# Kernel tuning notes

Measured on AMD Instinct MI355X. Metric: run time of the kernel, lower is better.

## Reference

```python
import jax, jax.numpy as jnp
import numpy as np

D_MODEL = 1024
NUM_HEADS = 16
D_K = D_MODEL // NUM_HEADS  # 64


def _xavier(key, shape):
    fan_in, fan_out = shape[-1], shape[-2]
    limit = float(np.sqrt(6.0 / (fan_in + fan_out)))
    return jax.random.uniform(key, shape, jnp.float32, -limit, limit)


def setup_inputs() -> dict:
    key = jax.random.key(0)
    kx, kq, kk, kv, ko = jax.random.split(key, 5)
    x = jax.random.normal(kx, (2, 2048, D_MODEL), dtype=jnp.float32)
    q_heads = _xavier(kq, (NUM_HEADS, D_K, D_MODEL))
    k_heads = _xavier(kk, (NUM_HEADS, D_K, D_MODEL))
    v_heads = _xavier(kv, (NUM_HEADS, D_K, D_MODEL))
    output_proj = _xavier(ko, (D_MODEL, NUM_HEADS * D_K))
    return {"x": x, "q_heads": q_heads, "k_heads": k_heads,
            "v_heads": v_heads, "output_proj": output_proj}


def reference(x, q_heads, k_heads, v_heads, output_proj):
    # x: [b, s, d]; q/k/v_heads: [h, dk, d]; output_proj: [d, h*dk]
    b, s, d = x.shape
    h, dk, _ = q_heads.shape
    scale = 1.0 / jnp.sqrt(jnp.asarray(dk, x.dtype))
    # per-head projections: [b, h, s, dk]
    Q = jnp.einsum('bsd,hkd->bhsk', x, q_heads)
    K = jnp.einsum('bsd,hkd->bhsk', x, k_heads)
    V = jnp.einsum('bsd,hkd->bhsk', x, v_heads)
    scores = jnp.einsum('bhqk,bhsk->bhqs', Q, K) * scale  # [b,h,s,s]
    causal = jnp.tril(jnp.ones((s, s), dtype=bool))       # True where allowed
    scores = jnp.where(causal, scores, -jnp.inf)
    attn = jax.nn.softmax(scores, axis=-1)
    out = jnp.einsum('bhqs,bhsk->bhqk', attn, V)           # [b,h,s,dk]
    out = out.transpose(0, 2, 1, 3).reshape(b, s, h * dk)  # [b,s,h*dk]
    return jnp.einsum('bsk,dk->bsd', out, output_proj)
```

## Files before the change

### kernel.cpp

```cpp
#include <hip/hip_runtime.h>
#include <hip/hip_bf16.h>
#include <math.h>

#define D_MODEL 1024
#define NHEADS  16
#define DK      64
#define SEQ     2048
#define KDIM    1024

typedef __bf16 bf16x8 __attribute__((ext_vector_type(8)));
typedef short  s16x4  __attribute__((ext_vector_type(4)));
typedef float  f32x4  __attribute__((ext_vector_type(4)));

__device__ __forceinline__ void gload16(const void* g, void* l) {
    __builtin_amdgcn_global_load_lds(
        (const __attribute__((address_space(1))) void*)g,
        (__attribute__((address_space(3))) void*)l, 16, 0, 0);
}

__device__ __forceinline__ unsigned short f2bf(float f) {
    __hip_bfloat16 h = __float2bfloat16(f);
    return *(unsigned short*)&h;
}

__device__ __forceinline__ unsigned pk2bf(float a, float b) {
    __hip_bfloat162 h = __float22bfloat162_rn(make_float2(a, b));
    return *(unsigned*)&h;
}

#define QSCALE 0.18033688011112042f

__global__ __launch_bounds__(256) void cast_kernel(
    const float* __restrict__ x,
    const float* __restrict__ qw,
    const float* __restrict__ kw,
    const float* __restrict__ vw,
    const float* __restrict__ wo,
    unsigned short* __restrict__ xb,
    unsigned short* __restrict__ wqkv,
    unsigned short* __restrict__ wob)
{
    const size_t t = (size_t)blockIdx.x * 256 + threadIdx.x;
    const size_t X4 = 1048576;
    const size_t W4 = 262144;

    const float* src;
    unsigned short* dst;
    size_t o;
    if (t < X4)            { src = x;  dst = xb;             o = t; }
    else if (t < X4 + W4)  { src = qw; dst = wqkv;           o = t - X4; }
    else if (t < X4 + 2*W4){ src = kw; dst = wqkv + 1048576; o = t - X4 - W4; }
    else if (t < X4 + 3*W4){ src = vw; dst = wqkv + 2097152; o = t - X4 - 2*W4; }
    else                   { src = wo; dst = wob;            o = t - X4 - 3*W4; }

    float4 v = ((const float4*)src)[o];
    ushort4 r;
    r.x = f2bf(v.x); r.y = f2bf(v.y); r.z = f2bf(v.z); r.w = f2bf(v.w);
    ((ushort4*)dst)[o] = r;
}

__global__ __launch_bounds__(256) void mfma_gemm_qkv(
    const unsigned short* __restrict__ A,
    const unsigned short* __restrict__ B,
    unsigned short* __restrict__ Qb,
    unsigned short* __restrict__ Kb,
    unsigned short* __restrict__ Vtb)
{
    __shared__ __align__(16) unsigned short smem[16384];
    unsigned short* As = smem;
    unsigned short* Bs = smem + 4096;

    const int tid  = threadIdx.x;
    const int wave = tid >> 6;
    const int lane = tid & 63;
    const int wr   = wave >> 1;
    const int wc   = wave & 1;
    const int quad = lane >> 4;
    const int l16  = lane & 15;

    const int rowBase = blockIdx.y * 128;
    const int colBase = blockIdx.x * 128;

    f32x4 acc[4][4];
    const f32x4 z = {0.f, 0.f, 0.f, 0.f};
#pragma unroll
    for (int i = 0; i < 4; ++i)
#pragma unroll
        for (int j = 0; j < 4; ++j) acc[i][j] = z;

    const int srow = lane >> 2;
    const int skof = (lane & 3) * 8;

    for (int k0 = 0; k0 < KDIM; k0 += 32) {
        __syncthreads();

        const unsigned short* ga =
            A + (size_t)(rowBase + wave * 32) * KDIM + k0;
        gload16(ga + (size_t)srow * KDIM + skof,        &As[(wave*32)    * 32]);
        gload16(ga + (size_t)(16 + srow) * KDIM + skof, &As[(wave*32+16) * 32]);

        const unsigned short* gb =
            B + (size_t)(colBase + wave * 32) * KDIM + k0;
        gload16(gb + (size_t)srow * KDIM + skof,        &Bs[(wave*32)    * 32]);
        gload16(gb + (size_t)(16 + srow) * KDIM + skof, &Bs[(wave*32+16) * 32]);

        __syncthreads();

        bf16x8 af[4], bfr[4];
#pragma unroll
        for (int t = 0; t < 4; ++t)
            af[t] = *(const bf16x8*)&As[(wr*64 + t*16 + l16) * 32 + quad*8];
#pragma unroll
        for (int t = 0; t < 4; ++t)
            bfr[t] = *(const bf16x8*)&Bs[(wc*64 + t*16 + l16) * 32 + quad*8];

#pragma unroll
        for (int tr = 0; tr < 4; ++tr)
#pragma unroll
            for (int tc = 0; tc < 4; ++tc)
                acc[tr][tc] = __builtin_amdgcn_mfma_f32_16x16x32_bf16(
                    af[tr], bfr[tc], acc[tr][tc], 0, 0, 0);
    }

    const int mat = colBase >> 10;
    const int b   = rowBase >> 11;
    const int sblk = rowBase & (SEQ - 1);
    __syncthreads();
    if (mat == 2) {
#pragma unroll
        for (int tr = 0; tr < 4; ++tr) {
#pragma unroll
            for (int tc = 0; tc < 4; ++tc) {
                const int col = wc*64 + tc*16 + l16;
#pragma unroll
                for (int reg = 0; reg < 4; ++reg) {
                    const int row = wr*64 + tr*16 + quad*4 + reg;
                    const int chunk = (row >> 3) ^ (col & 15);
                    smem[col*128 + chunk*8 + (row & 7)] = f2bf(acc[tr][tc][reg]);
                }
            }
        }
        __syncthreads();
        const int h0 = (colBase & 1023) >> 6;
#pragma unroll
        for (int i = 0; i < 8; ++i) {
            const int g  = i*256 + tid;
            const int kk = g >> 4;
            const int ci = g & 15;
            const int chunk = ci ^ (kk & 15);
            uint4 v = *(uint4*)&smem[kk*128 + chunk*8];
            const int h  = h0 + (kk >> 6), dk = kk & 63;
            *(uint4*)(Vtb + ((size_t)(b*NHEADS + h)*DK + dk)*SEQ + sblk + ci*8) = v;
        }
    } else {
        const float sc = (mat == 0) ? QSCALE : 1.0f;
#pragma unroll
        for (int tr = 0; tr < 4; ++tr) {
#pragma unroll
            for (int tc = 0; tc < 4; ++tc) {
                const int col   = wc*64 + tc*16 + l16;
                const int cbase = col >> 3, c7 = col & 7;
#pragma unroll
                for (int reg = 0; reg < 4; ++reg) {
                    const int row = wr*64 + tr*16 + quad*4 + reg;
                    const int chunk = cbase ^ (row & 15);
                    smem[row*128 + chunk*8 + c7] = f2bf(acc[tr][tc][reg] * sc);
                }
            }
        }
        __syncthreads();
        const int h0 = (colBase & 1023) >> 6;
        unsigned short* dstb = (mat == 0) ? Qb : Kb;
#pragma unroll
        for (int i = 0; i < 8; ++i) {
            const int g    = i*256 + tid;
            const int head = g >> 10;
            const int s    = (g >> 3) & 127;
            const int ci   = g & 7;
            const int chunk = (head*8 + ci) ^ (s & 15);
            uint4 v = *(uint4*)&smem[s*128 + chunk*8];
            *(uint4*)(dstb + ((size_t)(b*NHEADS + h0 + head)*SEQ + sblk + s)*DK
                           + ci*8) = v;
        }
    }
}

__global__ __launch_bounds__(256, 2) void attn_mfma_kernel(
    const unsigned short* __restrict__ Qb,
    const unsigned short* __restrict__ Kb,
    const unsigned short* __restrict__ Vtb,
    unsigned short* __restrict__ O)
{
    __shared__ unsigned short Ks[64 * 64];
    __shared__ unsigned short Vs[64 * 64];

    const int bh   = blockIdx.x;
    const int qt   = 31 - blockIdx.y;
    const int wave = threadIdx.x >> 6;
    const int lane = threadIdx.x & 63;
    const int quad = lane >> 4;
    const int l16  = lane & 15;

    const size_t qrow = (size_t)bh * SEQ + qt*64 + wave*16 + l16;
    bf16x8 aq0 = *(const bf16x8*)(Qb + qrow * DK + quad*8);
    bf16x8 aq1 = *(const bf16x8*)(Qb + qrow * DK + 32 + quad*8);

    f32x4 o_acc[4];
    const f32x4 z = {0.f, 0.f, 0.f, 0.f};
#pragma unroll
    for (int i = 0; i < 4; ++i) o_acc[i] = z;
    float lrow = 0.f;

    const int srow8  = lane >> 3;
    const int schunk = lane & 7;
    const unsigned short* Kbase = Kb  + (size_t)bh * SEQ * DK;
    const unsigned short* Vbase = Vtb + (size_t)bh * DK * SEQ;

    const int ntiles = qt + 1;
    for (int jt = 0; jt < ntiles; ++jt) {
        const int j0 = jt * 64;
        __syncthreads();
#pragma unroll
        for (int n = 0; n < 2; ++n) {
            const int r = wave*16 + n*8 + srow8;
            gload16(Kbase + (size_t)(j0 + r) * DK + (schunk ^ srow8) * 8,
                    &Ks[(wave*16 + n*8) * 64]);
            gload16(Vbase + (size_t)r * SEQ + j0 + (schunk ^ srow8) * 8,
                    &Vs[(wave*16 + n*8) * 64]);
        }
        __syncthreads();

        f32x4 st[4];
#pragma unroll
        for (int ct = 0; ct < 4; ++ct) {
            const int r = ct*16 + l16;
            bf16x8 k0 = *(const bf16x8*)&Ks[r*64 + ((quad     ^ (r&7)) * 8)];
            bf16x8 k1 = *(const bf16x8*)&Ks[r*64 + (((4+quad) ^ (r&7)) * 8)];
            f32x4 t = z;
            t = __builtin_amdgcn_mfma_f32_16x16x32_bf16(k0, aq0, t, 0, 0, 0);
            t = __builtin_amdgcn_mfma_f32_16x16x32_bf16(k1, aq1, t, 0, 0, 0);
            st[ct] = t;
        }

        if (jt == qt) {
#pragma unroll
            for (int ct = 0; ct < 4; ++ct)
#pragma unroll
                for (int reg = 0; reg < 4; ++reg) {
                    const int kl = ct*16 + quad*4 + reg;
                    const int ql = wave*16 + l16;
                    if (kl > ql) st[ct][reg] = -1e30f;
                }
        }

        float rs = 0.f;
#pragma unroll
        for (int ct = 0; ct < 4; ++ct)
#pragma unroll
            for (int reg = 0; reg < 4; ++reg) {
                float p = exp2f(st[ct][reg]);
                st[ct][reg] = p;
                rs += p;
            }
        rs += __shfl_xor(rs, 16);
        rs += __shfl_xor(rs, 32);
        lrow += rs;

        s16x4 pf[4];
#pragma unroll
        for (int ct = 0; ct < 4; ++ct) {
            union { unsigned u[2]; s16x4 s; } cv;
            cv.u[0] = pk2bf(st[ct][0], st[ct][1]);
            cv.u[1] = pk2bf(st[ct][2], st[ct][3]);
            pf[ct] = cv.s;
        }

#pragma unroll
        for (int ot = 0; ot < 4; ++ot) {
            const int r = ot*16 + l16;
#pragma unroll
            for (int ct = 0; ct < 4; ++ct) {
                const int cix = ct*2 + (quad >> 1);
                s16x4 vf = *(const s16x4*)&Vs[r*64 + ((cix ^ (r&7)) << 3)
                                              + (quad & 1) * 4];
                o_acc[ot] = __builtin_amdgcn_mfma_f32_16x16x16bf16_1k(
                    vf, pf[ct], o_acc[ot], 0, 0, 0);
            }
        }
    }

    const float inv = 1.f / lrow;
    const int b = bh >> 4, h = bh & 15;
    const int sg = qt*64 + wave*16 + l16;
    unsigned short* orow = O + ((size_t)(b * SEQ + sg)) * D_MODEL + h * DK;
#pragma unroll
    for (int ot = 0; ot < 4; ++ot) {
        uint2 pk;
        pk.x = pk2bf(o_acc[ot][0] * inv, o_acc[ot][1] * inv);
        pk.y = pk2bf(o_acc[ot][2] * inv, o_acc[ot][3] * inv);
        *(uint2*)(orow + ot*16 + quad*4) = pk;
    }
}

__global__ __launch_bounds__(256) void mfma_gemm_out(
    const unsigned short* __restrict__ A,
    const unsigned short* __restrict__ B,
    float* __restrict__ C0)
{
    __shared__ __align__(16) unsigned short As[64 * 32];
    __shared__ __align__(16) unsigned short Bs[128 * 32];

    const int tid  = threadIdx.x;
    const int wave = tid >> 6;
    const int lane = tid & 63;
    const int wr   = wave & 1;
    const int wc   = wave >> 1;
    const int quad = lane >> 4;
    const int l16  = lane & 15;

    const int rowBase = blockIdx.y * 64;
    const int colBase = blockIdx.x * 128;

    f32x4 acc[2][4];
    const f32x4 z = {0.f, 0.f, 0.f, 0.f};
#pragma unroll
    for (int i = 0; i < 2; ++i)
#pragma unroll
        for (int j = 0; j < 4; ++j) acc[i][j] = z;

    const int srow = lane >> 2;
    const int skof = (lane & 3) * 8;

    for (int k0 = 0; k0 < KDIM; k0 += 32) {
        __syncthreads();

        const unsigned short* ga =
            A + (size_t)(rowBase + wave * 16) * KDIM + k0;
        gload16(ga + (size_t)srow * KDIM + skof, &As[(wave*16) * 32]);

        const unsigned short* gb =
            B + (size_t)(colBase + wave * 32) * KDIM + k0;
        gload16(gb + (size_t)srow * KDIM + skof,        &Bs[(wave*32)    * 32]);
        gload16(gb + (size_t)(16 + srow) * KDIM + skof, &Bs[(wave*32+16) * 32]);

        __syncthreads();

        bf16x8 af[2], bfr[4];
#pragma unroll
        for (int t = 0; t < 2; ++t)
            af[t] = *(const bf16x8*)&As[(wr*32 + t*16 + l16) * 32 + quad*8];
#pragma unroll
        for (int t = 0; t < 4; ++t)
            bfr[t] = *(const bf16x8*)&Bs[(wc*64 + t*16 + l16) * 32 + quad*8];

#pragma unroll
        for (int tr = 0; tr < 2; ++tr)
#pragma unroll
            for (int tc = 0; tc < 4; ++tc)
                acc[tr][tc] = __builtin_amdgcn_mfma_f32_16x16x32_bf16(
                    af[tr], bfr[tc], acc[tr][tc], 0, 0, 0);
    }

#pragma unroll
    for (int tr = 0; tr < 2; ++tr) {
#pragma unroll
        for (int tc = 0; tc < 4; ++tc) {
            const int grow0 = rowBase + wr*32 + tr*16 + quad*4;
            const int gcol  = colBase + wc*64 + tc*16 + l16;
#pragma unroll
            for (int reg = 0; reg < 4; ++reg)
                C0[(size_t)(grow0 + reg) * D_MODEL + gcol] = acc[tr][tc][reg];
        }
    }
}

extern "C" void kernel_launch(void* const* d_in, const int* in_sizes, int n_in,
                              void* d_out, int out_size, void* d_ws, size_t ws_size,
                              hipStream_t stream) {
    const float* x  = (const float*)d_in[0];
    const float* qw = (const float*)d_in[1];
    const float* kw = (const float*)d_in[2];
    const float* vw = (const float*)d_in[3];
    const float* wo = (const float*)d_in[4];
    float* out = (float*)d_out;

    char* ws = (char*)d_ws;
    unsigned short* Qb   = (unsigned short*)(ws);
    unsigned short* Kb   = (unsigned short*)(ws + (size_t) 8*1024*1024);
    unsigned short* Vtb  = (unsigned short*)(ws + (size_t)16*1024*1024);
    unsigned short* AO   = (unsigned short*)(ws + (size_t)24*1024*1024);
    unsigned short* XB   = (unsigned short*)(ws + (size_t)32*1024*1024);
    unsigned short* WQKV = (unsigned short*)(ws + (size_t)40*1024*1024);
    unsigned short* WOB  = (unsigned short*)(ws + (size_t)46*1024*1024);

    cast_kernel<<<8192, 256, 0, stream>>>(x, qw, kw, vw, wo, XB, WQKV, WOB);

    dim3 g1(24, 32);
    mfma_gemm_qkv<<<g1, 256, 0, stream>>>(XB, WQKV, Qb, Kb, Vtb);

    dim3 g2(32, 32);
    attn_mfma_kernel<<<g2, 256, 0, stream>>>(Qb, Kb, Vtb, AO);

    dim3 g3(8, 64);
    mfma_gemm_out<<<g3, 256, 0, stream>>>(AO, WOB, out);
}
```

Before: 172.9 us.

## Double-buffer K/V tiles in LDS to prefetch next tile during compute

The attention kernel now keeps two LDS buffers each for K and V. It issues the async global-to-LDS loads for tile jt+1 right after the loop barrier, while the MFMA work on tile jt proceeds. This drops one of the two barriers per iteration and is meant to hide global load latency behind the score and PV computation. In exchange it doubles the attention kernel's LDS footprint. The overlap may also be lost if the compiler inserts a conservative vmcnt wait before the LDS reads.

```diff
diff --git a/kernel.cpp b/kernel.cpp
--- a/kernel.cpp
+++ b/kernel.cpp
@@ -191,8 +191,8 @@
     const unsigned short* __restrict__ Vtb,
     unsigned short* __restrict__ O)
 {
-    __shared__ unsigned short Ks[64 * 64];
-    __shared__ unsigned short Vs[64 * 64];
+    __shared__ unsigned short Ks[2][64 * 64];
+    __shared__ unsigned short Vs[2][64 * 64];
 
     const int bh   = blockIdx.x;
     const int qt   = 31 - blockIdx.y;
@@ -217,25 +217,40 @@
     const unsigned short* Vbase = Vtb + (size_t)bh * DK * SEQ;
 
     const int ntiles = qt + 1;
+
+#pragma unroll
+    for (int n = 0; n < 2; ++n) {
+        const int r = wave*16 + n*8 + srow8;
+        gload16(Kbase + (size_t)r * DK + (schunk ^ srow8) * 8,
+                &Ks[0][(wave*16 + n*8) * 64]);
+        gload16(Vbase + (size_t)r * SEQ + (schunk ^ srow8) * 8,
+                &Vs[0][(wave*16 + n*8) * 64]);
+    }
+
+    int bsel = 0;
     for (int jt = 0; jt < ntiles; ++jt) {
-        const int j0 = jt * 64;
-        __syncthreads();
-#pragma unroll
-        for (int n = 0; n < 2; ++n) {
-            const int r = wave*16 + n*8 + srow8;
-            gload16(Kbase + (size_t)(j0 + r) * DK + (schunk ^ srow8) * 8,
-                    &Ks[(wave*16 + n*8) * 64]);
-            gload16(Vbase + (size_t)r * SEQ + j0 + (schunk ^ srow8) * 8,
-                    &Vs[(wave*16 + n*8) * 64]);
-        }
-        __syncthreads();
+        __syncthreads();
+        if (jt + 1 < ntiles) {
+            const int j1 = (jt + 1) * 64;
+#pragma unroll
+            for (int n = 0; n < 2; ++n) {
+                const int r = wave*16 + n*8 + srow8;
+                gload16(Kbase + (size_t)(j1 + r) * DK + (schunk ^ srow8) * 8,
+                        &Ks[bsel ^ 1][(wave*16 + n*8) * 64]);
+                gload16(Vbase + (size_t)r * SEQ + j1 + (schunk ^ srow8) * 8,
+                        &Vs[bsel ^ 1][(wave*16 + n*8) * 64]);
+            }
+        }
+
+        const unsigned short* Kc = Ks[bsel];
+        const unsigned short* Vc = Vs[bsel];
 
         f32x4 st[4];
 #pragma unroll
         for (int ct = 0; ct < 4; ++ct) {
             const int r = ct*16 + l16;
-            bf16x8 k0 = *(const bf16x8*)&Ks[r*64 + ((quad     ^ (r&7)) * 8)];
-            bf16x8 k1 = *(const bf16x8*)&Ks[r*64 + (((4+quad) ^ (r&7)) * 8)];
+            bf16x8 k0 = *(const bf16x8*)&Kc[r*64 + ((quad     ^ (r&7)) * 8)];
+            bf16x8 k1 = *(const bf16x8*)&Kc[r*64 + (((4+quad) ^ (r&7)) * 8)];
             f32x4 t = z;
             t = __builtin_amdgcn_mfma_f32_16x16x32_bf16(k0, aq0, t, 0, 0, 0);
             t = __builtin_amdgcn_mfma_f32_16x16x32_bf16(k1, aq1, t, 0, 0, 0);
@@ -281,12 +296,13 @@
 #pragma unroll
             for (int ct = 0; ct < 4; ++ct) {
                 const int cix = ct*2 + (quad >> 1);
-                s16x4 vf = *(const s16x4*)&Vs[r*64 + ((cix ^ (r&7)) << 3)
+                s16x4 vf = *(const s16x4*)&Vc[r*64 + ((cix ^ (r&7)) << 3)
                                               + (quad & 1) * 4];
                 o_acc[ot] = __builtin_amdgcn_mfma_f32_16x16x16bf16_1k(
                     vf, pf[ct], o_acc[ot], 0, 0, 0);
             }
         }
+        bsel ^= 1;
     }
 
     const float inv = 1.f / lrow;
```

New measurement: 175.2 us. Within noise of the previous version (+1.3%).
